# Kernel optimization log

Hardware: AMD Instinct MI355X
Metric: run time of the kernel (lower is better)

The kernel has to match this reference:

```python
import jax, jax.numpy as jnp
import numpy as np
import math

B, C, H, W = 8, 64, 64, 64

def setup_inputs() -> dict:
    key = jax.random.key(0)
    k1, k2 = jax.random.split(key)
    x1 = jax.random.normal(k1, (B, C, H, W), dtype=jnp.float32)
    x2 = jax.random.normal(k2, (B, C, H, W), dtype=jnp.float32)
    return {"x1": x1, "x2": x2}

def reference(x1, x2):
    b, c, h, w = x1.shape
    # flatten spatial dims -> tokens: [B, HW, C]
    x1f = x1.reshape(b, c, h * w).transpose(0, 2, 1)
    x2f = x2.reshape(b, c, h * w).transpose(0, 2, 1)
    scale = 1.0 / math.sqrt(c)
    # direction A: queries from x1, keys/values from x2
    scores_a = jnp.einsum('bqc,bkc->bqk', x1f, x2f) * scale  # [B, HW, HW]
    out_a = jnp.einsum('bqk,bkc->bqc', jax.nn.softmax(scores_a, axis=-1), x2f)
    # direction B: queries from x2, keys/values from x1
    scores_b = jnp.einsum('bqc,bkc->bqk', x2f, x1f) * scale
    out_b = jnp.einsum('bqk,bkc->bqc', jax.nn.softmax(scores_b, axis=-1), x1f)
    out = (out_a + out_b).transpose(0, 2, 1).reshape(b, c, h, w)
    return out
```

## Files before the change

kernel.cpp:

```cpp
#include <hip/hip_runtime.h>
#include <hip/hip_bf16.h>
#include <stdint.h>


#define TT 4096
#define CC 64
#define NB 8

typedef float f32x4 __attribute__((ext_vector_type(4)));
typedef float f32x4a __attribute__((ext_vector_type(4), may_alias));
typedef short s16x8 __attribute__((ext_vector_type(8)));
typedef unsigned int u32x2a __attribute__((ext_vector_type(2), may_alias));
typedef unsigned int u32x4a __attribute__((ext_vector_type(4), may_alias));
typedef float f32a __attribute__((may_alias));

static __device__ __forceinline__ unsigned fbits(float x) { return __float_as_uint(x); }
static __device__ __forceinline__ ushort bf16of(float v) {
    return (ushort)((fbits(v) + 0x8000u) >> 16);
}
static __device__ __forceinline__ unsigned pack2(float a, float b) {
    return __builtin_amdgcn_perm(fbits(b) + 0x8000u, fbits(a) + 0x8000u, 0x07060302u);
}
static __device__ __forceinline__ s16x8 load_frag(const void* p) {
    u32x4a t = *(const u32x4a*)p;
    return __builtin_bit_cast(s16x8, t);
}

#define SQC1 0.4246609177f

__global__ void prep_k(const float* __restrict__ x1, const float* __restrict__ x2,
                       ushort* __restrict__ kt, ushort* __restrict__ vt) {
    const int inp = blockIdx.z, b = blockIdx.y, tt = blockIdx.x;
    const float* src = (inp == 0 ? x1 : x2) + (size_t)b * CC * TT;
    const size_t plane = (size_t)TT * CC;
    ushort* kd = kt + (size_t)(inp * NB + b) * plane;
    ushort* vd = vt + (size_t)(inp * NB + b) * plane;
    __shared__ ushort lds[64][72];
    const int tid = threadIdx.x;
    const int c  = tid >> 2;
    const int tg = tid & 3;
    const float* srow = src + (size_t)c * TT + tt * 64 + tg * 16;
    unsigned hw[8];
#pragma unroll
    for (int i = 0; i < 4; ++i) {
        f32x4a v = *(const f32x4a*)(srow + i * 4);
        hw[2 * i]     = pack2(v[0], v[1]);
        hw[2 * i + 1] = pack2(v[2], v[3]);
#pragma unroll
        for (int k = 0; k < 4; ++k) lds[tg * 16 + i * 4 + k][c] = bf16of(v[k] * SQC1);
    }
    {
        ushort* vchunk = vd + (((size_t)tt * 2 + (tg >> 1)) * 4 + (c >> 4)) * 512;
        const int l16v = c & 15;
        const int q0v  = (tg & 1) * 2;
        u32x4a w0 = {hw[0], hw[1], hw[2], hw[3]};
        u32x4a w1 = {hw[4], hw[5], hw[6], hw[7]};
        *(u32x4a*)(vchunk + (size_t)(q0v * 16 + l16v) * 8)       = w0;
        *(u32x4a*)(vchunk + (size_t)((q0v + 1) * 16 + l16v) * 8) = w1;
    }
    __syncthreads();
    const int mt   = tid >> 6;
    const int quad = (tid >> 4) & 3;
    const int l16  = tid & 15;
    const int t    = mt * 16 + l16;
#pragma unroll
    for (int ch = 0; ch < 2; ++ch) {
        u32x4a w = *(const u32x4a*)&lds[t][ch * 32 + quad * 8];
        *(u32x4a*)(kd + (((size_t)tt * 4 + mt) * 2 + ch) * 512 +
                   (size_t)(quad * 16 + l16) * 8) = w;
    }
}

__global__ __attribute__((amdgpu_flat_work_group_size(512, 512)))
void attn_fused_k(const ushort* __restrict__ kt, const ushort* __restrict__ vt,
                  float* __restrict__ out) {
    const int b    = blockIdx.x & 7;
    const int qt   = blockIdx.x >> 3;
    const int tid  = threadIdx.x;
    const int wave = tid >> 6;
    const int lane = tid & 63;
    const int quad = lane >> 4;
    const int l16  = lane & 15;
    const int dir  = wave & 1;
    const int pair = (wave >> 1) & 1;
    const int ks   = wave >> 2;
    const int q0   = qt * 64 + pair * 32;

    const size_t plane = (size_t)TT * CC;
    const ushort* Qp = kt + (size_t)((dir == 0 ? 0 : NB) + b) * plane + (size_t)lane * 8;
    const ushort* Kp = kt + (size_t)((dir == 0 ? NB : 0) + b) * plane + (size_t)lane * 8;
    const ushort* Vp = vt + (size_t)((dir == 0 ? NB : 0) + b) * plane + (size_t)lane * 8;

    __shared__ __align__(16) ushort pbuf[8][2][16][72];
    __shared__ float lpx[8][2][16];
    f32a* xbuf = (f32a*)&pbuf[0][0][0][0];

    s16x8 qf[2][2];
#pragma unroll
    for (int rb = 0; rb < 2; ++rb)
#pragma unroll
        for (int ch = 0; ch < 2; ++ch)
            qf[rb][ch] = load_frag(Qp + (((size_t)qt * 4 + pair * 2 + rb) * 2 + ch) * 512);

    f32x4 accO[2][4];
#pragma unroll
    for (int rb = 0; rb < 2; ++rb)
#pragma unroll
        for (int ct = 0; ct < 4; ++ct) accO[rb][ct] = (f32x4){0.f, 0.f, 0.f, 0.f};
    float lp[2] = {0.f, 0.f};

    s16x8 kA0, kA1, kA2, kA3, kA4, kA5, kA6, kA7;
    s16x8 kB0, kB1, kB2, kB3, kB4, kB5, kB6, kB7;
    s16x8 v0, v1, v2, v3, v4, v5, v6, v7;

    auto loadKA = [&](int j) {
        const ushort* p = Kp + (size_t)(ks * 32 + j) * 4096;
        kA0 = load_frag(p);          kA1 = load_frag(p + 512);
        kA2 = load_frag(p + 1024);   kA3 = load_frag(p + 1536);
        kA4 = load_frag(p + 2048);   kA5 = load_frag(p + 2560);
        kA6 = load_frag(p + 3072);   kA7 = load_frag(p + 3584);
    };
    auto loadKB = [&](int j) {
        const ushort* p = Kp + (size_t)(ks * 32 + j) * 4096;
        kB0 = load_frag(p);          kB1 = load_frag(p + 512);
        kB2 = load_frag(p + 1024);   kB3 = load_frag(p + 1536);
        kB4 = load_frag(p + 2048);   kB5 = load_frag(p + 2560);
        kB6 = load_frag(p + 3072);   kB7 = load_frag(p + 3584);
    };
    auto loadV = [&](int j) {
        const ushort* p = Vp + (size_t)(ks * 32 + j) * 4096;
        v0 = load_frag(p);           v1 = load_frag(p + 512);
        v2 = load_frag(p + 1024);    v3 = load_frag(p + 1536);
        v4 = load_frag(p + 2048);    v5 = load_frag(p + 2560);
        v6 = load_frag(p + 3072);    v7 = load_frag(p + 3584);
    };

    auto SmT = [&](s16x8 kc0, s16x8 kc1, int mt) {
#pragma unroll
        for (int rb = 0; rb < 2; ++rb) {
            f32x4 s = (f32x4){0.f, 0.f, 0.f, 0.f};
            s = __builtin_amdgcn_mfma_f32_16x16x32_bf16(kc0, qf[rb][0], s, 0, 0, 0);
            s = __builtin_amdgcn_mfma_f32_16x16x32_bf16(kc1, qf[rb][1], s, 0, 0, 0);
            float p0 = __builtin_amdgcn_exp2f(s[0]);
            float p1 = __builtin_amdgcn_exp2f(s[1]);
            float p2 = __builtin_amdgcn_exp2f(s[2]);
            float p3 = __builtin_amdgcn_exp2f(s[3]);
            lp[rb] += (p0 + p1) + (p2 + p3);
            u32x2a w;
            w[0] = pack2(p0, p1);
            w[1] = pack2(p2, p3);
            *(u32x2a*)&pbuf[wave][rb][l16][mt * 16 + quad * 4] = w;
        }
    };
    auto PVphase = [&]() {
        s16x8 pf0a = load_frag(&pbuf[wave][0][l16][quad * 8]);
        s16x8 pf1a = load_frag(&pbuf[wave][1][l16][quad * 8]);
        accO[0][0] = __builtin_amdgcn_mfma_f32_16x16x32_bf16(v0, pf0a, accO[0][0], 0, 0, 0);
        accO[1][0] = __builtin_amdgcn_mfma_f32_16x16x32_bf16(v0, pf1a, accO[1][0], 0, 0, 0);
        accO[0][1] = __builtin_amdgcn_mfma_f32_16x16x32_bf16(v1, pf0a, accO[0][1], 0, 0, 0);
        accO[1][1] = __builtin_amdgcn_mfma_f32_16x16x32_bf16(v1, pf1a, accO[1][1], 0, 0, 0);
        accO[0][2] = __builtin_amdgcn_mfma_f32_16x16x32_bf16(v2, pf0a, accO[0][2], 0, 0, 0);
        accO[1][2] = __builtin_amdgcn_mfma_f32_16x16x32_bf16(v2, pf1a, accO[1][2], 0, 0, 0);
        accO[0][3] = __builtin_amdgcn_mfma_f32_16x16x32_bf16(v3, pf0a, accO[0][3], 0, 0, 0);
        accO[1][3] = __builtin_amdgcn_mfma_f32_16x16x32_bf16(v3, pf1a, accO[1][3], 0, 0, 0);
        s16x8 pf0b = load_frag(&pbuf[wave][0][l16][32 + quad * 8]);
        s16x8 pf1b = load_frag(&pbuf[wave][1][l16][32 + quad * 8]);
        accO[0][0] = __builtin_amdgcn_mfma_f32_16x16x32_bf16(v4, pf0b, accO[0][0], 0, 0, 0);
        accO[1][0] = __builtin_amdgcn_mfma_f32_16x16x32_bf16(v4, pf1b, accO[1][0], 0, 0, 0);
        accO[0][1] = __builtin_amdgcn_mfma_f32_16x16x32_bf16(v5, pf0b, accO[0][1], 0, 0, 0);
        accO[1][1] = __builtin_amdgcn_mfma_f32_16x16x32_bf16(v5, pf1b, accO[1][1], 0, 0, 0);
        accO[0][2] = __builtin_amdgcn_mfma_f32_16x16x32_bf16(v6, pf0b, accO[0][2], 0, 0, 0);
        accO[1][2] = __builtin_amdgcn_mfma_f32_16x16x32_bf16(v6, pf1b, accO[1][2], 0, 0, 0);
        accO[0][3] = __builtin_amdgcn_mfma_f32_16x16x32_bf16(v7, pf0b, accO[0][3], 0, 0, 0);
        accO[1][3] = __builtin_amdgcn_mfma_f32_16x16x32_bf16(v7, pf1b, accO[1][3], 0, 0, 0);
    };

    loadKA(0);
    loadV(0);
#pragma unroll 1
    for (int j = 0; j < 32; j += 2) {
        loadKB(j + 1);
        SmT(kA0, kA1, 0); SmT(kA2, kA3, 1); SmT(kA4, kA5, 2); SmT(kA6, kA7, 3);
        PVphase();
        loadV(j + 1);
        if (j + 2 < 32) loadKA(j + 2);
        SmT(kB0, kB1, 0); SmT(kB2, kB3, 1); SmT(kB4, kB5, 2); SmT(kB6, kB7, 3);
        PVphase();
        if (j + 2 < 32) loadV(j + 2);
    }

    float inv[2];
#pragma unroll
    for (int rb = 0; rb < 2; ++rb) {
        float l = lp[rb];
        l += __shfl_xor(l, 16);
        l += __shfl_xor(l, 32);
        lp[rb] = l;
        if (lane < 16) lpx[wave][rb][l16] = l;
    }
    __syncthreads();
#pragma unroll
    for (int rb = 0; rb < 2; ++rb)
        inv[rb] = __builtin_amdgcn_rcpf(lp[rb] + lpx[wave ^ 4][rb][l16]);

    const int g = (ks << 1) | dir;
#pragma unroll 1
    for (int ph = 3; ph >= 1; --ph) {
        if (g == ph) {
#pragma unroll
            for (int rb = 0; rb < 2; ++rb)
#pragma unroll
                for (int ct = 0; ct < 4; ++ct)
#pragma unroll
                    for (int r = 0; r < 4; ++r) {
                        const int slot = (pair * 32 + rb * 16 + ct * 4 + r) * 64 + lane;
                        float v = accO[rb][ct][r] * inv[rb];
                        if (ph == 3) xbuf[slot] = v;
                        else xbuf[slot] += v;
                    }
        }
        __syncthreads();
    }
    if (g == 0) {
        float* ob = out + (size_t)b * plane;
#pragma unroll
        for (int rb = 0; rb < 2; ++rb)
#pragma unroll
            for (int ct = 0; ct < 4; ++ct)
#pragma unroll
                for (int r = 0; r < 4; ++r) {
                    float v = accO[rb][ct][r] * inv[rb] +
                              xbuf[(pair * 32 + rb * 16 + ct * 4 + r) * 64 + lane];
                    ob[(size_t)(ct * 16 + quad * 4 + r) * TT + q0 + rb * 16 + l16] = v;
                }
    }
}

extern "C" void kernel_launch(void* const* d_in, const int* in_sizes, int n_in,
                              void* d_out, int out_size, void* d_ws, size_t ws_size,
                              hipStream_t stream) {
    const float* x1 = (const float*)d_in[0];
    const float* x2 = (const float*)d_in[1];
    ushort* kt = (ushort*)d_ws;
    ushort* vt = (ushort*)d_ws + (size_t)2 * NB * TT * CC;

    hipLaunchKernelGGL(prep_k, dim3(TT / 64, NB, 2), dim3(256), 0, stream, x1, x2, kt, vt);
    hipLaunchKernelGGL(attn_fused_k, dim3(64 * NB), dim3(512), 0, stream,
                       kt, vt, (float*)d_out);
}
```

Before: 171.1 us.

## Double-buffer V fragments and P tiles to batch QK before PV

Splits the V register set and the per-wave LDS P buffer into two parities. Both key blocks' score/exp phases now run back to back, followed by both PV phases, so global loads of the next K/V are issued earlier and have more time to complete. This doubles LDS for P and adds eight more live VGPR fragments, which may raise register pressure and lower occupancy.

```diff
diff --git a/kernel.cpp b/kernel.cpp
--- a/kernel.cpp
+++ b/kernel.cpp
@@ -91,9 +91,9 @@
     const ushort* Kp = kt + (size_t)((dir == 0 ? NB : 0) + b) * plane + (size_t)lane * 8;
     const ushort* Vp = vt + (size_t)((dir == 0 ? NB : 0) + b) * plane + (size_t)lane * 8;
 
-    __shared__ __align__(16) ushort pbuf[8][2][16][72];
+    __shared__ __align__(16) ushort pbuf[8][2][2][16][72];
     __shared__ float lpx[8][2][16];
-    f32a* xbuf = (f32a*)&pbuf[0][0][0][0];
+    f32a* xbuf = (f32a*)&pbuf[0][0][0][0][0];
 
     s16x8 qf[2][2];
 #pragma unroll
@@ -111,7 +111,8 @@
 
     s16x8 kA0, kA1, kA2, kA3, kA4, kA5, kA6, kA7;
     s16x8 kB0, kB1, kB2, kB3, kB4, kB5, kB6, kB7;
-    s16x8 v0, v1, v2, v3, v4, v5, v6, v7;
+    s16x8 vA0, vA1, vA2, vA3, vA4, vA5, vA6, vA7;
+    s16x8 vB0, vB1, vB2, vB3, vB4, vB5, vB6, vB7;
 
     auto loadKA = [&](int j) {
         const ushort* p = Kp + (size_t)(ks * 32 + j) * 4096;
@@ -127,15 +128,22 @@
         kB4 = load_frag(p + 2048);   kB5 = load_frag(p + 2560);
         kB6 = load_frag(p + 3072);   kB7 = load_frag(p + 3584);
     };
-    auto loadV = [&](int j) {
+    auto loadVA = [&](int j) {
         const ushort* p = Vp + (size_t)(ks * 32 + j) * 4096;
-        v0 = load_frag(p);           v1 = load_frag(p + 512);
-        v2 = load_frag(p + 1024);    v3 = load_frag(p + 1536);
-        v4 = load_frag(p + 2048);    v5 = load_frag(p + 2560);
-        v6 = load_frag(p + 3072);    v7 = load_frag(p + 3584);
-    };
-
-    auto SmT = [&](s16x8 kc0, s16x8 kc1, int mt) {
+        vA0 = load_frag(p);          vA1 = load_frag(p + 512);
+        vA2 = load_frag(p + 1024);   vA3 = load_frag(p + 1536);
+        vA4 = load_frag(p + 2048);   vA5 = load_frag(p + 2560);
+        vA6 = load_frag(p + 3072);   vA7 = load_frag(p + 3584);
+    };
+    auto loadVB = [&](int j) {
+        const ushort* p = Vp + (size_t)(ks * 32 + j) * 4096;
+        vB0 = load_frag(p);          vB1 = load_frag(p + 512);
+        vB2 = load_frag(p + 1024);   vB3 = load_frag(p + 1536);
+        vB4 = load_frag(p + 2048);   vB5 = load_frag(p + 2560);
+        vB6 = load_frag(p + 3072);   vB7 = load_frag(p + 3584);
+    };
+
+    auto SmT = [&](s16x8 kc0, s16x8 kc1, int mt, int par) {
 #pragma unroll
         for (int rb = 0; rb < 2; ++rb) {
             f32x4 s = (f32x4){0.f, 0.f, 0.f, 0.f};
@@ -149,44 +157,66 @@
             u32x2a w;
             w[0] = pack2(p0, p1);
             w[1] = pack2(p2, p3);
-            *(u32x2a*)&pbuf[wave][rb][l16][mt * 16 + quad * 4] = w;
+            *(u32x2a*)&pbuf[wave][par][rb][l16][mt * 16 + quad * 4] = w;
         }
     };
-    auto PVphase = [&]() {
-        s16x8 pf0a = load_frag(&pbuf[wave][0][l16][quad * 8]);
-        s16x8 pf1a = load_frag(&pbuf[wave][1][l16][quad * 8]);
-        accO[0][0] = __builtin_amdgcn_mfma_f32_16x16x32_bf16(v0, pf0a, accO[0][0], 0, 0, 0);
-        accO[1][0] = __builtin_amdgcn_mfma_f32_16x16x32_bf16(v0, pf1a, accO[1][0], 0, 0, 0);
-        accO[0][1] = __builtin_amdgcn_mfma_f32_16x16x32_bf16(v1, pf0a, accO[0][1], 0, 0, 0);
-        accO[1][1] = __builtin_amdgcn_mfma_f32_16x16x32_bf16(v1, pf1a, accO[1][1], 0, 0, 0);
-        accO[0][2] = __builtin_amdgcn_mfma_f32_16x16x32_bf16(v2, pf0a, accO[0][2], 0, 0, 0);
-        accO[1][2] = __builtin_amdgcn_mfma_f32_16x16x32_bf16(v2, pf1a, accO[1][2], 0, 0, 0);
-        accO[0][3] = __builtin_amdgcn_mfma_f32_16x16x32_bf16(v3, pf0a, accO[0][3], 0, 0, 0);
-        accO[1][3] = __builtin_amdgcn_mfma_f32_16x16x32_bf16(v3, pf1a, accO[1][3], 0, 0, 0);
-        s16x8 pf0b = load_frag(&pbuf[wave][0][l16][32 + quad * 8]);
-        s16x8 pf1b = load_frag(&pbuf[wave][1][l16][32 + quad * 8]);
-        accO[0][0] = __builtin_amdgcn_mfma_f32_16x16x32_bf16(v4, pf0b, accO[0][0], 0, 0, 0);
-        accO[1][0] = __builtin_amdgcn_mfma_f32_16x16x32_bf16(v4, pf1b, accO[1][0], 0, 0, 0);
-        accO[0][1] = __builtin_amdgcn_mfma_f32_16x16x32_bf16(v5, pf0b, accO[0][1], 0, 0, 0);
-        accO[1][1] = __builtin_amdgcn_mfma_f32_16x16x32_bf16(v5, pf1b, accO[1][1], 0, 0, 0);
-        accO[0][2] = __builtin_amdgcn_mfma_f32_16x16x32_bf16(v6, pf0b, accO[0][2], 0, 0, 0);
-        accO[1][2] = __builtin_amdgcn_mfma_f32_16x16x32_bf16(v6, pf1b, accO[1][2], 0, 0, 0);
-        accO[0][3] = __builtin_amdgcn_mfma_f32_16x16x32_bf16(v7, pf0b, accO[0][3], 0, 0, 0);
-        accO[1][3] = __builtin_amdgcn_mfma_f32_16x16x32_bf16(v7, pf1b, accO[1][3], 0, 0, 0);
+    auto PVA = [&]() {
+        s16x8 pf0a = load_frag(&pbuf[wave][0][0][l16][quad * 8]);
+        s16x8 pf1a = load_frag(&pbuf[wave][0][1][l16][quad * 8]);
+        accO[0][0] = __builtin_amdgcn_mfma_f32_16x16x32_bf16(vA0, pf0a, accO[0][0], 0, 0, 0);
+        accO[1][0] = __builtin_amdgcn_mfma_f32_16x16x32_bf16(vA0, pf1a, accO[1][0], 0, 0, 0);
+        accO[0][1] = __builtin_amdgcn_mfma_f32_16x16x32_bf16(vA1, pf0a, accO[0][1], 0, 0, 0);
+        accO[1][1] = __builtin_amdgcn_mfma_f32_16x16x32_bf16(vA1, pf1a, accO[1][1], 0, 0, 0);
+        accO[0][2] = __builtin_amdgcn_mfma_f32_16x16x32_bf16(vA2, pf0a, accO[0][2], 0, 0, 0);
+        accO[1][2] = __builtin_amdgcn_mfma_f32_16x16x32_bf16(vA2, pf1a, accO[1][2], 0, 0, 0);
+        accO[0][3] = __builtin_amdgcn_mfma_f32_16x16x32_bf16(vA3, pf0a, accO[0][3], 0, 0, 0);
+        accO[1][3] = __builtin_amdgcn_mfma_f32_16x16x32_bf16(vA3, pf1a, accO[1][3], 0, 0, 0);
+        s16x8 pf0b = load_frag(&pbuf[wave][0][0][l16][32 + quad * 8]);
+        s16x8 pf1b = load_frag(&pbuf[wave][0][1][l16][32 + quad * 8]);
+        accO[0][0] = __builtin_amdgcn_mfma_f32_16x16x32_bf16(vA4, pf0b, accO[0][0], 0, 0, 0);
+        accO[1][0] = __builtin_amdgcn_mfma_f32_16x16x32_bf16(vA4, pf1b, accO[1][0], 0, 0, 0);
+        accO[0][1] = __builtin_amdgcn_mfma_f32_16x16x32_bf16(vA5, pf0b, accO[0][1], 0, 0, 0);
+        accO[1][1] = __builtin_amdgcn_mfma_f32_16x16x32_bf16(vA5, pf1b, accO[1][1], 0, 0, 0);
+        accO[0][2] = __builtin_amdgcn_mfma_f32_16x16x32_bf16(vA6, pf0b, accO[0][2], 0, 0, 0);
+        accO[1][2] = __builtin_amdgcn_mfma_f32_16x16x32_bf16(vA6, pf1b, accO[1][2], 0, 0, 0);
+        accO[0][3] = __builtin_amdgcn_mfma_f32_16x16x32_bf16(vA7, pf0b, accO[0][3], 0, 0, 0);
+        accO[1][3] = __builtin_amdgcn_mfma_f32_16x16x32_bf16(vA7, pf1b, accO[1][3], 0, 0, 0);
+    };
+    auto PVB = [&]() {
+        s16x8 pf0a = load_frag(&pbuf[wave][1][0][l16][quad * 8]);
+        s16x8 pf1a = load_frag(&pbuf[wave][1][1][l16][quad * 8]);
+        accO[0][0] = __builtin_amdgcn_mfma_f32_16x16x32_bf16(vB0, pf0a, accO[0][0], 0, 0, 0);
+        accO[1][0] = __builtin_amdgcn_mfma_f32_16x16x32_bf16(vB0, pf1a, accO[1][0], 0, 0, 0);
+        accO[0][1] = __builtin_amdgcn_mfma_f32_16x16x32_bf16(vB1, pf0a, accO[0][1], 0, 0, 0);
+        accO[1][1] = __builtin_amdgcn_mfma_f32_16x16x32_bf16(vB1, pf1a, accO[1][1], 0, 0, 0);
+        accO[0][2] = __builtin_amdgcn_mfma_f32_16x16x32_bf16(vB2, pf0a, accO[0][2], 0, 0, 0);
+        accO[1][2] = __builtin_amdgcn_mfma_f32_16x16x32_bf16(vB2, pf1a, accO[1][2], 0, 0, 0);
+        accO[0][3] = __builtin_amdgcn_mfma_f32_16x16x32_bf16(vB3, pf0a, accO[0][3], 0, 0, 0);
+        accO[1][3] = __builtin_amdgcn_mfma_f32_16x16x32_bf16(vB3, pf1a, accO[1][3], 0, 0, 0);
+        s16x8 pf0b = load_frag(&pbuf[wave][1][0][l16][32 + quad * 8]);
+        s16x8 pf1b = load_frag(&pbuf[wave][1][1][l16][32 + quad * 8]);
+        accO[0][0] = __builtin_amdgcn_mfma_f32_16x16x32_bf16(vB4, pf0b, accO[0][0], 0, 0, 0);
+        accO[1][0] = __builtin_amdgcn_mfma_f32_16x16x32_bf16(vB4, pf1b, accO[1][0], 0, 0, 0);
+        accO[0][1] = __builtin_amdgcn_mfma_f32_16x16x32_bf16(vB5, pf0b, accO[0][1], 0, 0, 0);
+        accO[1][1] = __builtin_amdgcn_mfma_f32_16x16x32_bf16(vB5, pf1b, accO[1][1], 0, 0, 0);
+        accO[0][2] = __builtin_amdgcn_mfma_f32_16x16x32_bf16(vB6, pf0b, accO[0][2], 0, 0, 0);
+        accO[1][2] = __builtin_amdgcn_mfma_f32_16x16x32_bf16(vB6, pf1b, accO[1][2], 0, 0, 0);
+        accO[0][3] = __builtin_amdgcn_mfma_f32_16x16x32_bf16(vB7, pf0b, accO[0][3], 0, 0, 0);
+        accO[1][3] = __builtin_amdgcn_mfma_f32_16x16x32_bf16(vB7, pf1b, accO[1][3], 0, 0, 0);
     };
 
     loadKA(0);
-    loadV(0);
+    loadVA(0);
 #pragma unroll 1
     for (int j = 0; j < 32; j += 2) {
         loadKB(j + 1);
-        SmT(kA0, kA1, 0); SmT(kA2, kA3, 1); SmT(kA4, kA5, 2); SmT(kA6, kA7, 3);
-        PVphase();
-        loadV(j + 1);
+        SmT(kA0, kA1, 0, 0); SmT(kA2, kA3, 1, 0); SmT(kA4, kA5, 2, 0); SmT(kA6, kA7, 3, 0);
+        loadVB(j + 1);
+        SmT(kB0, kB1, 0, 1); SmT(kB2, kB3, 1, 1); SmT(kB4, kB5, 2, 1); SmT(kB6, kB7, 3, 1);
         if (j + 2 < 32) loadKA(j + 2);
-        SmT(kB0, kB1, 0); SmT(kB2, kB3, 1); SmT(kB4, kB5, 2); SmT(kB6, kB7, 3);
-        PVphase();
-        if (j + 2 < 32) loadV(j + 2);
+        PVA();
+        if (j + 2 < 32) loadVA(j + 2);
+        PVB();
     }
 
     float inv[2];
```

New measurement: 163.6 us. -4.4%, faster.
